# Kernel optimization log

Measured on AMD Instinct MI355X. Metric: run time of the kernel, lower is better.

## Reference

```python
import jax, jax.numpy as jnp
import numpy as np

D_MODEL = 512
NUM_HEADS = 8


def setup_inputs() -> dict:
    key = jax.random.key(0)
    ks = jax.random.split(key, 6)
    B, S, D = 4, 2048, D_MODEL
    Q = jax.random.normal(ks[0], (B, S, D), dtype=jnp.float32)
    K = jax.random.normal(ks[1], (B, S, D), dtype=jnp.float32)
    V = jax.random.normal(ks[2], (B, S, D), dtype=jnp.float32)
    # boolean mask, True = masked out; random so no row is fully masked
    mask = jax.random.randint(ks[3], (B, S, S), 0, 2).astype(jnp.bool_)
    scale = 1.0 / np.sqrt(D)
    Wq = jax.random.normal(ks[4], (D, D), dtype=jnp.float32) * scale
    Wo = jax.random.normal(ks[5], (D, D), dtype=jnp.float32) * scale
    return {"Q": Q, "K": K, "V": V, "mask": mask, "Wq": Wq, "Wo": Wo}


def reference(Q, K, V, mask, Wq, Wo):
    B, S, D = Q.shape
    H = NUM_HEADS
    dk = D // H
    # Faithful to the source: Q_Linear's weight (Wq) is applied to Q, K AND V
    # (K_Linear / V_Linear are dead parameters in the original module).
    q = (Q @ Wq.T).reshape(B, S, H, dk)
    k = (K @ Wq.T).reshape(B, S, H, dk)
    v = (V @ Wq.T).reshape(B, S, H, dk)
    # scores: [B, H, Sq, Sk]
    scores = jnp.einsum("bqhd,bkhd->bhqk", q, k)
    scores = jnp.where(mask[:, None, :, :], -jnp.inf, scores)
    w = jax.nn.softmax(scores / jnp.sqrt(jnp.asarray(dk, scores.dtype)), axis=-1)
    c = jnp.einsum("bhqk,bkhd->bqhd", w, v).reshape(B, S, D)
    return c @ Wo.T
```

## Files before the change

kernel.cpp:

```cpp
#include <hip/hip_runtime.h>
#include <math.h>

#define B_ 4
#define S_ 2048
#define D_ 512
#define H_ 8
#define DK_ 64
#define MROWS (B_ * S_)

typedef short bf16x8 __attribute__((ext_vector_type(8)));
typedef short bf16x4 __attribute__((ext_vector_type(4)));
typedef float f32x4 __attribute__((ext_vector_type(4)));

static __device__ __forceinline__ unsigned short f2bf(float x) {
    unsigned int u = __float_as_uint(x);
    return (unsigned short)((u + 0x7FFFu + ((u >> 16) & 1u)) >> 16);
}
static __device__ __forceinline__ unsigned int cvt_pk_bf16(float a, float b) {
    unsigned int r;
    asm("v_cvt_pk_bf16_f32 %0, %1, %2" : "=v"(r) : "v"(a), "v"(b));
    return r;
}
static __device__ __forceinline__ float exp2_fast(float x) {
    float r;
    asm("v_exp_f32 %0, %1" : "=v"(r) : "v"(x));
    return r;
}
static __device__ __forceinline__ void gld_lds16(const unsigned short* g, unsigned short* l) {
    __builtin_amdgcn_global_load_lds(
        (const __attribute__((address_space(1))) unsigned int*)g,
        (__attribute__((address_space(3))) unsigned int*)l, 16, 0, 0);
}
static __device__ __forceinline__ f32x4 mfma16(bf16x4 a, bf16x4 b, f32x4 c) {
#if __has_builtin(__builtin_amdgcn_mfma_f32_16x16x16_bf16)
    return __builtin_amdgcn_mfma_f32_16x16x16_bf16(a, b, c, 0, 0, 0);
#elif __has_builtin(__builtin_amdgcn_mfma_f32_16x16x16bf16_1k)
    return __builtin_amdgcn_mfma_f32_16x16x16bf16_1k(a, b, c, 0, 0, 0);
#else
    f32x4 d;
    asm volatile("v_mfma_f32_16x16x16_bf16 %0, %1, %2, %0"
                 : "=v"(d) : "v"(a), "v"(b), "0"(c));
    return d;
#endif
}

#define NXE (MROWS * D_)
#define NWE (D_ * D_)
#define CAST_BLOCKS ((3 * NXE + 2 * NWE) / 8 / 256)
#define MASK_BLOCKS (B_ * S_ * S_ / 256)

__global__ __launch_bounds__(256) void prep(const float* __restrict__ Q,
                                            const float* __restrict__ K,
                                            const float* __restrict__ V,
                                            const float* __restrict__ Wq,
                                            const float* __restrict__ Wo,
                                            const void* __restrict__ mask,
                                            unsigned short* __restrict__ Qb,
                                            unsigned short* __restrict__ Kb,
                                            unsigned short* __restrict__ Vb,
                                            unsigned short* __restrict__ Wqb,
                                            unsigned short* __restrict__ Wob,
                                            unsigned long long* __restrict__ mb) {
    if (blockIdx.x < CAST_BLOCKS) {
        const int NA = NXE / 8;
        const int NWn = NWE / 8;
        int id = blockIdx.x * 256 + threadIdx.x;
        const float* src;
        unsigned short* dst;
        if (id < 3 * NA) {
            int a = id / NA, r = id - a * NA;
            src = (a == 0 ? Q : a == 1 ? K : V) + (size_t)r * 8;
            dst = (a == 0 ? Qb : a == 1 ? Kb : Vb) + (size_t)r * 8;
        } else {
            int r = id - 3 * NA;
            int a = r / NWn; r -= a * NWn;
            src = (a == 0 ? Wq : Wo) + (size_t)r * 8;
            dst = (a == 0 ? Wqb : Wob) + (size_t)r * 8;
        }
        float4 x = *(const float4*)src;
        float4 y = *(const float4*)(src + 4);
        unsigned short u[8] = {f2bf(x.x), f2bf(x.y), f2bf(x.z), f2bf(x.w),
                               f2bf(y.x), f2bf(y.y), f2bf(y.z), f2bf(y.w)};
        *(uint4*)dst = *(const uint4*)u;
    } else {
        const int id = (blockIdx.x - CAST_BLOCKS) * 256 + threadIdx.x;
        unsigned int accw = 0;
        if ((threadIdx.x & 63) == 0) {
            const unsigned int* mw0 = (const unsigned int*)mask;
            #pragma unroll
            for (int i = 0; i < 16; ++i) accw |= mw0[i];
        }
        accw = __shfl(accw, 0);
        const bool bytemode = (accw & 0xFFFFFF00u) != 0u;
        int val;
        if (bytemode) val = ((const unsigned char*)mask)[id];
        else          val = ((const int*)mask)[id];
        unsigned long long w = __ballot(val != 0);
        if ((threadIdx.x & 63) == 0) mb[id >> 6] = w;
    }
}

__global__ __launch_bounds__(256) void proj3(const unsigned short* __restrict__ Qb,
                                             const unsigned short* __restrict__ Kb,
                                             const unsigned short* __restrict__ Vb,
                                             const unsigned short* __restrict__ Wqb,
                                             unsigned short* __restrict__ qs,
                                             unsigned short* __restrict__ kbo,
                                             unsigned short* __restrict__ vt) {
    __shared__ unsigned short As[128 * 40];
    __shared__ unsigned short Bs[128 * 40];
    const int t = threadIdx.x;
    const int w = t >> 6, lane = t & 63, col = lane & 15, quad = lane >> 4;
    const int bm = blockIdx.x * 128, bn = blockIdx.y * 128;
    const int z = blockIdx.z;
    const unsigned short* X = (z == 0) ? Qb : (z == 1) ? Kb : Vb;
    const int wm = (w >> 1) * 64, wn = (w & 1) * 64;
    const int srow = t >> 1, shalf = t & 1;

    const unsigned short* xg = X + (size_t)(bm + srow) * D_ + shalf * 16;
    const unsigned short* wg = Wqb + (size_t)(bn + srow) * D_ + shalf * 16;
    unsigned short* asw = &As[srow * 40 + shalf * 16];
    unsigned short* bsw = &Bs[srow * 40 + shalf * 16];

    f32x4 acc[4][4];
    #pragma unroll
    for (int i = 0; i < 4; ++i)
        #pragma unroll
        for (int j = 0; j < 4; ++j) acc[i][j] = (f32x4){0.f, 0.f, 0.f, 0.f};

    #pragma unroll 1
    for (int k0 = 0; k0 < D_; k0 += 32) {
        __syncthreads();
        {
            uint4 a0 = *(const uint4*)(xg + k0);
            uint4 a1 = *(const uint4*)(xg + k0 + 8);
            uint4 b0 = *(const uint4*)(wg + k0);
            uint4 b1 = *(const uint4*)(wg + k0 + 8);
            *(uint4*)asw = a0; *(uint4*)(asw + 8) = a1;
            *(uint4*)bsw = b0; *(uint4*)(bsw + 8) = b1;
        }
        __syncthreads();

        bf16x8 af[4], bg[4];
        #pragma unroll
        for (int i = 0; i < 4; ++i)
            af[i] = *(const bf16x8*)&As[(wm + i * 16 + col) * 40 + quad * 8];
        #pragma unroll
        for (int j = 0; j < 4; ++j)
            bg[j] = *(const bf16x8*)&Bs[(wn + j * 16 + col) * 40 + quad * 8];
        #pragma unroll
        for (int i = 0; i < 4; ++i)
            #pragma unroll
            for (int j = 0; j < 4; ++j)
                acc[i][j] = __builtin_amdgcn_mfma_f32_16x16x32_bf16(
                    af[i], bg[j], acc[i][j], 0, 0, 0);
    }

    if (z == 2) {
        #pragma unroll
        for (int i = 0; i < 4; ++i) {
            const int R = bm + wm + i * 16 + quad * 4;
            const int bb = R >> 11, s0 = R & (S_ - 1);
            #pragma unroll
            for (int j = 0; j < 4; ++j) {
                const int C = bn + wn + j * 16 + col;
                const int hh = C >> 6, dd = C & (DK_ - 1);
                ushort4 u = make_ushort4(f2bf(acc[i][j][0]), f2bf(acc[i][j][1]),
                                         f2bf(acc[i][j][2]), f2bf(acc[i][j][3]));
                *(ushort4*)&vt[(((size_t)bb * H_ + hh) * DK_ + dd) * S_ + s0] = u;
            }
        }
    } else {
        unsigned short* O = (z == 0) ? qs : kbo;
        const float scl = (z == 0) ? 0.18033688f : 1.0f;
        #pragma unroll
        for (int i = 0; i < 4; ++i)
            #pragma unroll
            for (int j = 0; j < 4; ++j) {
                const int R = bm + wm + i * 16 + quad * 4;
                const int C = bn + wn + j * 16 + col;
                #pragma unroll
                for (int r = 0; r < 4; ++r)
                    O[(size_t)(R + r) * D_ + C] = f2bf(acc[i][j][r] * scl);
            }
    }
}

__global__ __launch_bounds__(256) void gemm_out(const unsigned short* __restrict__ Xb,
                                                const unsigned short* __restrict__ Wob,
                                                float* __restrict__ Out) {
    __shared__ unsigned short As[128 * 40];
    __shared__ unsigned short Bs[128 * 40];
    const int t = threadIdx.x;
    const int w = t >> 6, lane = t & 63, col = lane & 15, quad = lane >> 4;
    const int bm = blockIdx.x * 128, bn = blockIdx.y * 128;
    const int wm = (w >> 1) * 64, wn = (w & 1) * 64;
    const int srow = t >> 1, shalf = t & 1;

    const unsigned short* xg = Xb + (size_t)(bm + srow) * D_ + shalf * 16;
    const unsigned short* wg = Wob + (size_t)(bn + srow) * D_ + shalf * 16;
    unsigned short* asw = &As[srow * 40 + shalf * 16];
    unsigned short* bsw = &Bs[srow * 40 + shalf * 16];

    f32x4 acc[4][4];
    #pragma unroll
    for (int i = 0; i < 4; ++i)
        #pragma unroll
        for (int j = 0; j < 4; ++j) acc[i][j] = (f32x4){0.f, 0.f, 0.f, 0.f};

    #pragma unroll 1
    for (int k0 = 0; k0 < D_; k0 += 32) {
        __syncthreads();
        {
            uint4 a0 = *(const uint4*)(xg + k0);
            uint4 a1 = *(const uint4*)(xg + k0 + 8);
            uint4 b0 = *(const uint4*)(wg + k0);
            uint4 b1 = *(const uint4*)(wg + k0 + 8);
            *(uint4*)asw = a0; *(uint4*)(asw + 8) = a1;
            *(uint4*)bsw = b0; *(uint4*)(bsw + 8) = b1;
        }
        __syncthreads();

        bf16x8 af[4], bg[4];
        #pragma unroll
        for (int i = 0; i < 4; ++i)
            af[i] = *(const bf16x8*)&As[(wm + i * 16 + col) * 40 + quad * 8];
        #pragma unroll
        for (int j = 0; j < 4; ++j)
            bg[j] = *(const bf16x8*)&Bs[(wn + j * 16 + col) * 40 + quad * 8];
        #pragma unroll
        for (int i = 0; i < 4; ++i)
            #pragma unroll
            for (int j = 0; j < 4; ++j)
                acc[i][j] = __builtin_amdgcn_mfma_f32_16x16x32_bf16(
                    af[i], bg[j], acc[i][j], 0, 0, 0);
    }

    #pragma unroll
    for (int i = 0; i < 4; ++i)
        #pragma unroll
        for (int j = 0; j < 4; ++j) {
            const int R = bm + wm + i * 16 + quad * 4;
            const int C = bn + wn + j * 16 + col;
            #pragma unroll
            for (int r = 0; r < 4; ++r)
                Out[(size_t)(R + r) * D_ + C] = acc[i][j][r];
        }
}

__global__ __launch_bounds__(256, 4) void attn_mfma(
        const unsigned short* __restrict__ qb,
        const unsigned short* __restrict__ kb,
        const unsigned short* __restrict__ vt,
        const unsigned long long* __restrict__ mb,
        unsigned short* __restrict__ o0,
        unsigned short* __restrict__ o1,
        float* __restrict__ l0,
        float* __restrict__ l1) {
    __shared__ unsigned short sm[16384];
    const int t = threadIdx.x;
    const int w = t >> 6;
    const int lane = t & 63;
    const int col = lane & 15;
    const int quad = lane >> 4;
    const int h = blockIdx.y;
    const int b = blockIdx.z >> 1;
    const int khalf = blockIdx.z & 1;
    const int bh = b * H_ + h;
    const int qrow0 = blockIdx.x * 128 + w * 32;

    unsigned short* opart = khalf ? o1 : o0;
    float* lpart = khalf ? l1 : l0;

    const unsigned int chk = cvt_pk_bf16(1.0f, 2.0f);
    const bool ablow = ((chk & 0xFFFFu) == 0x3F80u);

    bf16x8 aQ0[2], aQ1[2];
    #pragma unroll
    for (int s = 0; s < 2; ++s) {
        const unsigned short* qp =
            qb + (size_t)(b * S_ + qrow0 + s * 16 + col) * D_ + h * DK_ + quad * 8;
        aQ0[s] = *(const bf16x8*)(qp);
        aQ1[s] = *(const bf16x8*)(qp + 32);
    }

    bf16x4 ones4;
    #pragma unroll
    for (int i = 0; i < 4; ++i) ones4[i] = (short)0x3F80;

    f32x4 O[2][4];
    #pragma unroll
    for (int s = 0; s < 2; ++s)
        #pragma unroll
        for (int g = 0; g < 4; ++g) O[s][g] = (f32x4){0.f, 0.f, 0.f, 0.f};
    f32x4 lacc[2];
    lacc[0] = (f32x4){0.f, 0.f, 0.f, 0.f};
    lacc[1] = (f32x4){0.f, 0.f, 0.f, 0.f};

    const float CREF = 8.656170245f;
    const int kbeg = khalf * (S_ / 2);

    const int ln8 = lane >> 3;
    const int fs8 = ((lane & 7) ^ ln8) * 8;
    const int r0 = w * 16 + ln8;
    const unsigned short* pK0 = kb + (size_t)(b * S_ + kbeg + r0) * D_ + h * DK_ + fs8;
    const unsigned short* pK1 = pK0 + 8 * D_;
    const unsigned short* pV0 = vt + ((size_t)bh * DK_ + r0) * S_ + kbeg + fs8;
    const unsigned short* pV1 = pV0 + 8 * S_;

    const unsigned long long* mbase0 =
        mb + (size_t)(b * S_ + qrow0 + col) * (S_ / 64) + (kbeg >> 6);
    const unsigned long long* mbase1 = mbase0 + 16 * (S_ / 64);

    gld_lds16(pK0, &sm[w * 1024]);
    gld_lds16(pK1, &sm[w * 1024 + 512]);
    gld_lds16(pV0, &sm[4096 + w * 1024]);
    gld_lds16(pV1, &sm[4096 + w * 1024 + 512]);
    pK0 += 64 * D_; pK1 += 64 * D_; pV0 += 64; pV1 += 64;

    const int c7 = col & 7;
    const int ps0 = (quad ^ c7) * 8;
    const int ps1 = ps0 ^ 32;
    const int vq = quad >> 1;
    const int vr = (quad & 1) * 4;

    #pragma unroll 1
    for (int ti = 0; ti < 16; ++ti) {
        unsigned long long mw0 = mbase0[ti];
        unsigned long long mw1 = mbase1[ti];
        __builtin_amdgcn_sched_barrier(0);
        if (ti < 15) {
            const int nb = (ti & 1) ? 0 : 8192;
            gld_lds16(pK0, &sm[nb + w * 1024]);
            gld_lds16(pK1, &sm[nb + w * 1024 + 512]);
            gld_lds16(pV0, &sm[nb + 4096 + w * 1024]);
            gld_lds16(pV1, &sm[nb + 4096 + w * 1024 + 512]);
            pK0 += 64 * D_; pK1 += 64 * D_; pV0 += 64; pV1 += 64;
            __asm__ __volatile__("s_waitcnt vmcnt(6)" ::: "memory");
        } else {
            __asm__ __volatile__("s_waitcnt vmcnt(2)" ::: "memory");
        }
        __builtin_amdgcn_s_barrier();

        const int KB = (ti & 1) ? 8192 : 0;
        const int VB = KB + 4096;

        f32x4 sc[2][4];
        __builtin_amdgcn_s_setprio(1);
        #pragma unroll
        for (int g = 0; g < 4; ++g) {
            const int krow = KB + (g * 16 + col) * 64;
            bf16x8 bk0 = *(const bf16x8*)&sm[krow + ps0];
            bf16x8 bk1 = *(const bf16x8*)&sm[krow + ps1];
            #pragma unroll
            for (int s = 0; s < 2; ++s) {
                f32x4 z = {0.f, 0.f, 0.f, 0.f};
                z = __builtin_amdgcn_mfma_f32_16x16x32_bf16(bk0, aQ0[s], z, 0, 0, 0);
                z = __builtin_amdgcn_mfma_f32_16x16x32_bf16(bk1, aQ1[s], z, 0, 0, 0);
                sc[s][g] = z;
            }
        }
        __builtin_amdgcn_s_setprio(0);

        bf16x4 pf[2][4];
        #pragma unroll
        for (int s = 0; s < 2; ++s) {
            const unsigned long long mws = s ? mw1 : mw0;
            #pragma unroll
            for (int g = 0; g < 4; ++g) {
                const unsigned int m4 =
                    (unsigned int)(mws >> (g * 16 + quad * 4)) & 0xFu;
                float p0 = exp2_fast(((m4 & 1u) ? -1e30f : sc[s][g][0]) - CREF);
                float p1 = exp2_fast(((m4 & 2u) ? -1e30f : sc[s][g][1]) - CREF);
                float p2 = exp2_fast(((m4 & 4u) ? -1e30f : sc[s][g][2]) - CREF);
                float p3 = exp2_fast(((m4 & 8u) ? -1e30f : sc[s][g][3]) - CREF);
                const unsigned int w0 = ablow ? cvt_pk_bf16(p0, p1)
                                              : cvt_pk_bf16(p1, p0);
                const unsigned int w1 = ablow ? cvt_pk_bf16(p2, p3)
                                              : cvt_pk_bf16(p3, p2);
                union { unsigned long long u; bf16x4 v; } cv;
                cv.u = (unsigned long long)w0 | ((unsigned long long)w1 << 32);
                pf[s][g] = cv.v;
            }
        }

        __builtin_amdgcn_s_setprio(1);
        #pragma unroll
        for (int s = 0; s < 2; ++s)
            #pragma unroll
            for (int g = 0; g < 4; ++g)
                lacc[s] = mfma16(pf[s][g], ones4, lacc[s]);

        #pragma unroll
        for (int g = 0; g < 4; ++g) {
            const int vx = VB + ((2 * g + vq) ^ c7) * 8 + vr;
            #pragma unroll
            for (int db = 0; db < 4; ++db) {
                bf16x4 vf = *(const bf16x4*)&sm[vx + (db * 16 + col) * 64];
                #pragma unroll
                for (int s = 0; s < 2; ++s)
                    O[s][db] = mfma16(pf[s][g], vf, O[s][db]);
            }
        }
        __builtin_amdgcn_s_setprio(0);

        __builtin_amdgcn_s_barrier();
    }

    #pragma unroll
    for (int s = 0; s < 2; ++s)
        #pragma unroll
        for (int r = 0; r < 4; ++r) {
            const int row = b * S_ + qrow0 + s * 16 + quad * 4 + r;
            #pragma unroll
            for (int g = 0; g < 4; ++g)
                opart[(size_t)row * D_ + h * DK_ + g * 16 + col] = f2bf(O[s][g][r]);
            if (col == 0) lpart[(size_t)row * H_ + h] = lacc[s][r];
        }
}

__global__ __launch_bounds__(256) void combine(const unsigned short* __restrict__ o0,
                                               const unsigned short* __restrict__ o1,
                                               const float* __restrict__ l0,
                                               const float* __restrict__ l1,
                                               unsigned short* __restrict__ cb) {
    const int id = blockIdx.x * 256 + threadIdx.x;
    const size_t base = (size_t)id * 8;
    const int row = (int)(base >> 9);
    const int hh = ((int)base & (D_ - 1)) >> 6;
    uint4 ua = *(const uint4*)(o0 + base);
    uint4 ub = *(const uint4*)(o1 + base);
    const float inv = 1.0f / (l0[(size_t)row * H_ + hh] + l1[(size_t)row * H_ + hh]);
    const unsigned short* pa = (const unsigned short*)&ua;
    const unsigned short* pb = (const unsigned short*)&ub;
    unsigned short out[8];
    #pragma unroll
    for (int i = 0; i < 8; ++i) {
        float fa = __uint_as_float((unsigned int)pa[i] << 16);
        float fb = __uint_as_float((unsigned int)pb[i] << 16);
        out[i] = f2bf((fa + fb) * inv);
    }
    *(uint4*)(cb + base) = *(const uint4*)out;
}

extern "C" void kernel_launch(void* const* d_in, const int* in_sizes, int n_in,
                              void* d_out, int out_size, void* d_ws, size_t ws_size,
                              hipStream_t stream) {
    const float* Q    = (const float*)d_in[0];
    const float* K    = (const float*)d_in[1];
    const float* V    = (const float*)d_in[2];
    const void*  mask = d_in[3];
    const float* Wq   = (const float*)d_in[4];
    const float* Wo   = (const float*)d_in[5];
    float* out = (float*)d_out;

    const size_t NX = (size_t)MROWS * D_;
    const size_t NW = (size_t)D_ * D_;
    unsigned short* Qb   = (unsigned short*)d_ws;
    unsigned short* Kb   = Qb + NX;
    unsigned short* Vb   = Kb + NX;
    unsigned short* Wqb  = Vb + NX;
    unsigned short* Wob  = Wqb + NW;
    unsigned short* qbuf = Wob + NW;
    unsigned short* kbuf = qbuf + NX;
    unsigned short* vtb  = kbuf + NX;
    unsigned short* cbuf = vtb + NX;
    unsigned long long* mb = (unsigned long long*)(cbuf + NX);

    unsigned short* o0 = Qb;
    unsigned short* o1 = Kb;
    float* l0 = (float*)Vb;
    float* l1 = l0 + (size_t)MROWS * H_;

    prep<<<dim3(CAST_BLOCKS + MASK_BLOCKS), dim3(256), 0, stream>>>(
        Q, K, V, Wq, Wo, mask, Qb, Kb, Vb, Wqb, Wob, mb);

    proj3<<<dim3(MROWS / 128, D_ / 128, 3), dim3(256), 0, stream>>>(
        Qb, Kb, Vb, Wqb, qbuf, kbuf, vtb);

    attn_mfma<<<dim3(S_ / 128, H_, B_ * 2), dim3(256), 0, stream>>>(
        qbuf, kbuf, vtb, mb, o0, o1, l0, l1);

    combine<<<dim3((int)(NX / 8 / 256)), dim3(256), 0, stream>>>(o0, o1, l0, l1, cbuf);

    gemm_out<<<dim3(MROWS / 128, D_ / 128), dim3(256), 0, stream>>>(cbuf, Wob, out);
}
```

Before: 277.1 us.

## Switch attention kernel to 32x32x16 MFMA tiles with permlane-swapped P operands

Rewrites the attention inner loop to use 32x32x16 bf16 MFMA instructions instead of 16x16x32/16x16x16, with each wave computing 32 keys by 32 queries per instruction. The probability tile is converted into the A-operand layout in registers using v_permlane32_swap, which avoids an LDS round trip. Mask loading collapses to one 64-bit word per lane. The aim is to issue fewer, larger matrix instructions and fewer LDS fragment loads per tile. In exchange it uses larger accumulators and adds cross-lane swaps, which may raise register pressure under launch_bounds(256,4).

```diff
diff --git a/kernel.cpp b/kernel.cpp
--- a/kernel.cpp
+++ b/kernel.cpp
@@ -11,6 +11,7 @@
 typedef short bf16x8 __attribute__((ext_vector_type(8)));
 typedef short bf16x4 __attribute__((ext_vector_type(4)));
 typedef float f32x4 __attribute__((ext_vector_type(4)));
+typedef float f32x16 __attribute__((ext_vector_type(16)));
 
 static __device__ __forceinline__ unsigned short f2bf(float x) {
     unsigned int u = __float_as_uint(x);
@@ -31,17 +32,8 @@
         (const __attribute__((address_space(1))) unsigned int*)g,
         (__attribute__((address_space(3))) unsigned int*)l, 16, 0, 0);
 }
-static __device__ __forceinline__ f32x4 mfma16(bf16x4 a, bf16x4 b, f32x4 c) {
-#if __has_builtin(__builtin_amdgcn_mfma_f32_16x16x16_bf16)
-    return __builtin_amdgcn_mfma_f32_16x16x16_bf16(a, b, c, 0, 0, 0);
-#elif __has_builtin(__builtin_amdgcn_mfma_f32_16x16x16bf16_1k)
-    return __builtin_amdgcn_mfma_f32_16x16x16bf16_1k(a, b, c, 0, 0, 0);
-#else
-    f32x4 d;
-    asm volatile("v_mfma_f32_16x16x16_bf16 %0, %1, %2, %0"
-                 : "=v"(d) : "v"(a), "v"(b), "0"(c));
-    return d;
-#endif
+static __device__ __forceinline__ void plswap(unsigned int& a, unsigned int& b) {
+    asm volatile("v_permlane32_swap_b32 %0, %1" : "+v"(a), "+v"(b));
 }
 
 #define NXE (MROWS * D_)
@@ -261,8 +253,8 @@
     const int t = threadIdx.x;
     const int w = t >> 6;
     const int lane = t & 63;
-    const int col = lane & 15;
-    const int quad = lane >> 4;
+    const int q5 = lane & 31;
+    const int hi = lane >> 5;
     const int h = blockIdx.y;
     const int b = blockIdx.z >> 1;
     const int khalf = blockIdx.z & 1;
@@ -275,27 +267,22 @@
     const unsigned int chk = cvt_pk_bf16(1.0f, 2.0f);
     const bool ablow = ((chk & 0xFFFFu) == 0x3F80u);
 
-    bf16x8 aQ0[2], aQ1[2];
-    #pragma unroll
-    for (int s = 0; s < 2; ++s) {
+    bf16x8 qf[4];
+    {
         const unsigned short* qp =
-            qb + (size_t)(b * S_ + qrow0 + s * 16 + col) * D_ + h * DK_ + quad * 8;
-        aQ0[s] = *(const bf16x8*)(qp);
-        aQ1[s] = *(const bf16x8*)(qp + 32);
-    }
-
-    bf16x4 ones4;
-    #pragma unroll
-    for (int i = 0; i < 4; ++i) ones4[i] = (short)0x3F80;
-
-    f32x4 O[2][4];
-    #pragma unroll
-    for (int s = 0; s < 2; ++s)
-        #pragma unroll
-        for (int g = 0; g < 4; ++g) O[s][g] = (f32x4){0.f, 0.f, 0.f, 0.f};
-    f32x4 lacc[2];
-    lacc[0] = (f32x4){0.f, 0.f, 0.f, 0.f};
-    lacc[1] = (f32x4){0.f, 0.f, 0.f, 0.f};
+            qb + (size_t)(b * S_ + qrow0 + q5) * D_ + h * DK_ + hi * 8;
+        #pragma unroll
+        for (int dsl = 0; dsl < 4; ++dsl)
+            qf[dsl] = *(const bf16x8*)(qp + dsl * 16);
+    }
+
+    bf16x8 ones8;
+    #pragma unroll
+    for (int i = 0; i < 8; ++i) ones8[i] = (short)0x3F80;
+
+    f32x16 Oa, Ob, lacc;
+    #pragma unroll
+    for (int i = 0; i < 16; ++i) { Oa[i] = 0.f; Ob[i] = 0.f; lacc[i] = 0.f; }
 
     const float CREF = 8.656170245f;
     const int kbeg = khalf * (S_ / 2);
@@ -308,9 +295,8 @@
     const unsigned short* pV0 = vt + ((size_t)bh * DK_ + r0) * S_ + kbeg + fs8;
     const unsigned short* pV1 = pV0 + 8 * S_;
 
-    const unsigned long long* mbase0 =
-        mb + (size_t)(b * S_ + qrow0 + col) * (S_ / 64) + (kbeg >> 6);
-    const unsigned long long* mbase1 = mbase0 + 16 * (S_ / 64);
+    const unsigned long long* mbase =
+        mb + (size_t)(b * S_ + qrow0 + q5) * (S_ / 64) + (kbeg >> 6);
 
     gld_lds16(pK0, &sm[w * 1024]);
     gld_lds16(pK1, &sm[w * 1024 + 512]);
@@ -318,16 +304,11 @@
     gld_lds16(pV1, &sm[4096 + w * 1024 + 512]);
     pK0 += 64 * D_; pK1 += 64 * D_; pV0 += 64; pV1 += 64;
 
-    const int c7 = col & 7;
-    const int ps0 = (quad ^ c7) * 8;
-    const int ps1 = ps0 ^ 32;
-    const int vq = quad >> 1;
-    const int vr = (quad & 1) * 4;
+    const int x7 = (q5 & 7);
 
     #pragma unroll 1
     for (int ti = 0; ti < 16; ++ti) {
-        unsigned long long mw0 = mbase0[ti];
-        unsigned long long mw1 = mbase1[ti];
+        unsigned long long mw = mbase[ti];
         __builtin_amdgcn_sched_barrier(0);
         if (ti < 15) {
             const int nb = (ti & 1) ? 0 : 8192;
@@ -336,87 +317,77 @@
             gld_lds16(pV0, &sm[nb + 4096 + w * 1024]);
             gld_lds16(pV1, &sm[nb + 4096 + w * 1024 + 512]);
             pK0 += 64 * D_; pK1 += 64 * D_; pV0 += 64; pV1 += 64;
-            __asm__ __volatile__("s_waitcnt vmcnt(6)" ::: "memory");
+            __asm__ __volatile__("s_waitcnt vmcnt(5)" ::: "memory");
         } else {
-            __asm__ __volatile__("s_waitcnt vmcnt(2)" ::: "memory");
+            __asm__ __volatile__("s_waitcnt vmcnt(1)" ::: "memory");
         }
         __builtin_amdgcn_s_barrier();
 
         const int KB = (ti & 1) ? 8192 : 0;
         const int VB = KB + 4096;
-
-        f32x4 sc[2][4];
-        __builtin_amdgcn_s_setprio(1);
-        #pragma unroll
-        for (int g = 0; g < 4; ++g) {
-            const int krow = KB + (g * 16 + col) * 64;
-            bf16x8 bk0 = *(const bf16x8*)&sm[krow + ps0];
-            bf16x8 bk1 = *(const bf16x8*)&sm[krow + ps1];
-            #pragma unroll
-            for (int s = 0; s < 2; ++s) {
-                f32x4 z = {0.f, 0.f, 0.f, 0.f};
-                z = __builtin_amdgcn_mfma_f32_16x16x32_bf16(bk0, aQ0[s], z, 0, 0, 0);
-                z = __builtin_amdgcn_mfma_f32_16x16x32_bf16(bk1, aQ1[s], z, 0, 0, 0);
-                sc[s][g] = z;
+        const unsigned long long msh = mw >> (hi * 4);
+
+        #pragma unroll
+        for (int kbi = 0; kbi < 2; ++kbi) {
+            const int krow = KB + (kbi * 32 + q5) * 64;
+            f32x16 S;
+            #pragma unroll
+            for (int i = 0; i < 16; ++i) S[i] = 0.f;
+            __builtin_amdgcn_s_setprio(1);
+            #pragma unroll
+            for (int dsl = 0; dsl < 4; ++dsl) {
+                bf16x8 kf = *(const bf16x8*)&sm[krow + (((dsl << 1) | hi) ^ x7) * 8];
+                S = __builtin_amdgcn_mfma_f32_32x32x16_bf16(kf, qf[dsl], S, 0, 0, 0);
             }
-        }
-        __builtin_amdgcn_s_setprio(0);
-
-        bf16x4 pf[2][4];
-        #pragma unroll
-        for (int s = 0; s < 2; ++s) {
-            const unsigned long long mws = s ? mw1 : mw0;
-            #pragma unroll
-            for (int g = 0; g < 4; ++g) {
-                const unsigned int m4 =
-                    (unsigned int)(mws >> (g * 16 + quad * 4)) & 0xFu;
-                float p0 = exp2_fast(((m4 & 1u) ? -1e30f : sc[s][g][0]) - CREF);
-                float p1 = exp2_fast(((m4 & 2u) ? -1e30f : sc[s][g][1]) - CREF);
-                float p2 = exp2_fast(((m4 & 4u) ? -1e30f : sc[s][g][2]) - CREF);
-                float p3 = exp2_fast(((m4 & 8u) ? -1e30f : sc[s][g][3]) - CREF);
-                const unsigned int w0 = ablow ? cvt_pk_bf16(p0, p1)
-                                              : cvt_pk_bf16(p1, p0);
-                const unsigned int w1 = ablow ? cvt_pk_bf16(p2, p3)
-                                              : cvt_pk_bf16(p3, p2);
-                union { unsigned long long u; bf16x4 v; } cv;
-                cv.u = (unsigned long long)w0 | ((unsigned long long)w1 << 32);
-                pf[s][g] = cv.v;
+            __builtin_amdgcn_s_setprio(0);
+
+            float p[16];
+            #pragma unroll
+            for (int r = 0; r < 16; ++r) {
+                const int c = kbi * 32 + (r & 3) + 8 * (r >> 2);
+                const bool msk = ((msh >> c) & 1ull) != 0ull;
+                p[r] = exp2_fast((msk ? -1e30f : S[r]) - CREF);
             }
-        }
-
-        __builtin_amdgcn_s_setprio(1);
-        #pragma unroll
-        for (int s = 0; s < 2; ++s)
-            #pragma unroll
-            for (int g = 0; g < 4; ++g)
-                lacc[s] = mfma16(pf[s][g], ones4, lacc[s]);
-
-        #pragma unroll
-        for (int g = 0; g < 4; ++g) {
-            const int vx = VB + ((2 * g + vq) ^ c7) * 8 + vr;
-            #pragma unroll
-            for (int db = 0; db < 4; ++db) {
-                bf16x4 vf = *(const bf16x4*)&sm[vx + (db * 16 + col) * 64];
-                #pragma unroll
-                for (int s = 0; s < 2; ++s)
-                    O[s][db] = mfma16(pf[s][g], vf, O[s][db]);
+
+            #pragma unroll
+            for (int ksl = 0; ksl < 2; ++ksl) {
+                const int bsl = ksl * 8;
+                unsigned int uA = ablow ? cvt_pk_bf16(p[bsl], p[bsl + 1])
+                                        : cvt_pk_bf16(p[bsl + 1], p[bsl]);
+                unsigned int uB = ablow ? cvt_pk_bf16(p[bsl + 2], p[bsl + 3])
+                                        : cvt_pk_bf16(p[bsl + 3], p[bsl + 2]);
+                unsigned int uC = ablow ? cvt_pk_bf16(p[bsl + 4], p[bsl + 5])
+                                        : cvt_pk_bf16(p[bsl + 5], p[bsl + 4]);
+                unsigned int uD = ablow ? cvt_pk_bf16(p[bsl + 6], p[bsl + 7])
+                                        : cvt_pk_bf16(p[bsl + 7], p[bsl + 6]);
+                plswap(uA, uC);
+                plswap(uB, uD);
+                union { unsigned int u[4]; bf16x8 v; } pa;
+                pa.u[0] = uA; pa.u[1] = uB; pa.u[2] = uC; pa.u[3] = uD;
+
+                const int slice = kbi * 2 + ksl;
+                const int vseg = (((slice << 1) | hi) ^ x7) * 8;
+                bf16x8 vf0 = *(const bf16x8*)&sm[VB + q5 * 64 + vseg];
+                bf16x8 vf1 = *(const bf16x8*)&sm[VB + (32 + q5) * 64 + vseg];
+                __builtin_amdgcn_s_setprio(1);
+                lacc = __builtin_amdgcn_mfma_f32_32x32x16_bf16(pa.v, ones8, lacc, 0, 0, 0);
+                Oa = __builtin_amdgcn_mfma_f32_32x32x16_bf16(pa.v, vf0, Oa, 0, 0, 0);
+                Ob = __builtin_amdgcn_mfma_f32_32x32x16_bf16(pa.v, vf1, Ob, 0, 0, 0);
+                __builtin_amdgcn_s_setprio(0);
             }
         }
-        __builtin_amdgcn_s_setprio(0);
 
         __builtin_amdgcn_s_barrier();
     }
 
     #pragma unroll
-    for (int s = 0; s < 2; ++s)
-        #pragma unroll
-        for (int r = 0; r < 4; ++r) {
-            const int row = b * S_ + qrow0 + s * 16 + quad * 4 + r;
-            #pragma unroll
-            for (int g = 0; g < 4; ++g)
-                opart[(size_t)row * D_ + h * DK_ + g * 16 + col] = f2bf(O[s][g][r]);
-            if (col == 0) lpart[(size_t)row * H_ + h] = lacc[s][r];
-        }
+    for (int r = 0; r < 16; ++r) {
+        const int qq = (r & 3) + 8 * (r >> 2) + 4 * hi;
+        const size_t row = (size_t)(b * S_ + qrow0 + qq);
+        opart[row * D_ + h * DK_ + q5]      = f2bf(Oa[r]);
+        opart[row * D_ + h * DK_ + 32 + q5] = f2bf(Ob[r]);
+        if (q5 == 0) lpart[row * H_ + h] = lacc[r];
+    }
 }
 
 __global__ __launch_bounds__(256) void combine(const unsigned short* __restrict__ o0,
```

New measurement: 281.0 us. About the same (+1.4%).
